# Optimization experiments

Measured on AMD Instinct MI355X. Metric: run time of the kernel, lower is better.

## Reference

```python
import jax, jax.numpy as jnp
import numpy as np

B, L, H, C = 1, 512, 1024, 2


def setup_inputs() -> dict:
    key = jax.random.key(0)
    k1, k2, k3 = jax.random.split(key, 3)
    lm_output = jax.random.normal(k1, (B, L, H), dtype=jnp.float32)
    # torch Linear weight layout: [out_features, in_features]
    W1 = jax.random.normal(k2, (H, 2 * H), dtype=jnp.float32) * 0.02
    b1 = jnp.zeros((H,), dtype=jnp.float32)
    W2 = jax.random.normal(k3, (C, H), dtype=jnp.float32) * 0.02
    b2 = jnp.zeros((C,), dtype=jnp.float32)
    return {"lm_output": lm_output, "W1": W1, "b1": b1, "W2": W2, "b2": b2}


def reference(lm_output, W1, b1, W2, b2):
    # pair_emb[b,i,j] = concat(lm_output[b,j], lm_output[b,i])
    # Linear(concat(a,b)) decomposes: split W1 into the halves acting on each part.
    Wa = W1[:, :H]  # acts on lm_output_a (the j / column token)
    Wb = W1[:, H:]  # acts on lm_output_b (the i / row token)
    a_proj = jnp.einsum('blh,oh->blo', lm_output, Wa)  # [B,L,H]
    b_proj = jnp.einsum('blh,oh->blo', lm_output, Wb)  # [B,L,H]
    # hidden[b,i,j] = tanh(a_proj[b,j] + b_proj[b,i] + b1)   -> [B,L,L,H]
    hidden = jnp.tanh(a_proj[:, None, :, :] + b_proj[:, :, None, :] + b1)
    # Dropout is identity at inference time.
    logits = jnp.einsum('bijh,ch->bijc', hidden, W2) + b2  # [B,L,L,C]
    logits = (logits + jnp.swapaxes(logits, 1, 2)) / 2.0
    return logits
```

## Files before the change

### kernel.cpp

```cpp
#include <hip/hip_runtime.h>
#include <hip/hip_bf16.h>

#define HH 1024
#define LL 512
#define TNT 8
#define NTILE 36

typedef __attribute__((ext_vector_type(8))) short bf16x8;
typedef __attribute__((ext_vector_type(4))) float f32x4;
typedef __attribute__((ext_vector_type(2))) float f32x2;

static constexpr float C_EXP = 2.8853900817779268f;

static __device__ __forceinline__ uint4 pack8(f32x4 a, f32x4 b) {
    union { uint4 u; __hip_bfloat162 h[4]; } r;
    r.h[0] = __float22bfloat162_rn(make_float2(a.x, a.y));
    r.h[1] = __float22bfloat162_rn(make_float2(a.z, a.w));
    r.h[2] = __float22bfloat162_rn(make_float2(b.x, b.y));
    r.h[3] = __float22bfloat162_rn(make_float2(b.z, b.w));
    return r.u;
}

static __device__ __forceinline__ f32x2 lo2(f32x4 v) { return __builtin_shufflevector(v, v, 0, 1); }
static __device__ __forceinline__ f32x2 hi2(f32x4 v) { return __builtin_shufflevector(v, v, 2, 3); }

__global__ __launch_bounds__(256, 4) void proj_mfma_kernel(
    const float* __restrict__ lm, const float* __restrict__ W1,
    const float* __restrict__ b1, float* __restrict__ Ea, float* __restrict__ Eb)
{
    __shared__ ushort As[64][136];
    __shared__ ushort Bs[32][136];

    const int tid  = threadIdx.x;
    const int lane = tid & 63;
    const int w    = tid >> 6;
    const int b    = blockIdx.x;
    const int xcd  = b & 7;
    const int idx  = b >> 3;
    const int nbase = (xcd * 8 + (idx & 7)) * 32;
    const int mbase = (idx >> 3) * 64;
    const int wm   = w * 16;
    const int sel  = nbase >> 10;
    const int nrow = nbase & 1023;

    const int frow = lane & 15;
    const int q8   = (lane >> 4) * 8;

    f32x4 acc[2] = {};

    for (int kb = 0; kb < HH; kb += 128) {
        __syncthreads();
        {
            int p = tid;
#pragma unroll
            for (int it = 0; it < 4; ++it, p += 256) {
                const int row = p >> 4, c8 = (p & 15) * 8;
                const float* pa = &lm[(mbase + row) * HH + kb + c8];
                *(uint4*)&As[row][c8] = pack8(*(const f32x4*)pa, *(const f32x4*)(pa + 4));
            }
            int q = tid;
#pragma unroll
            for (int it = 0; it < 2; ++it, q += 256) {
                const int row = q >> 4, c8 = (q & 15) * 8;
                const float* pw = &W1[(nrow + row) * 2048 + sel * 1024 + kb + c8];
                *(uint4*)&Bs[row][c8] = pack8(*(const f32x4*)pw, *(const f32x4*)(pw + 4));
            }
        }
        __syncthreads();

#pragma unroll
        for (int s = 0; s < 4; ++s) {
            const bf16x8 a = *(const bf16x8*)&As[wm + frow][s * 32 + q8];
#pragma unroll
            for (int nf = 0; nf < 2; ++nf) {
                const bf16x8 bb = *(const bf16x8*)&Bs[nf * 16 + frow][s * 32 + q8];
                acc[nf] = __builtin_amdgcn_mfma_f32_16x16x32_bf16(a, bb, acc[nf], 0, 0, 0);
            }
        }
    }

    const int col = lane & 15;
    const int rq  = (lane >> 4) * 4;
    const int m0  = mbase + wm + rq;
    const bool isA = sel == 0;
#pragma unroll
    for (int nf = 0; nf < 2; ++nf) {
        const int nn = (nrow + nf * 16 + col);
        if (isA) {
            const float bb = b1[nn];
#pragma unroll
            for (int r = 0; r < 4; ++r)
                Ea[(m0 + r) * HH + nn] = __builtin_amdgcn_exp2f(C_EXP * (acc[nf][r] + bb));
        } else {
#pragma unroll
            for (int r = 0; r < 4; ++r)
                Eb[(m0 + r) * HH + nn] = __builtin_amdgcn_exp2f(C_EXP * acc[nf][r]);
        }
    }
}

__global__ __launch_bounds__(256, 3) void pair_kernel(
    const float* __restrict__ Ea, const float* __restrict__ Eb,
    const float* __restrict__ W2, float* __restrict__ pbuf, int slice)
{
    __shared__ float tl[4][64][32];

    const int tid = threadIdx.x;
    const int tx  = tid & 15;
    const int ty  = tid >> 4;

    int tt = blockIdx.x, bi = 0, rem = TNT;
    while (tt >= rem) { tt -= rem; --rem; ++bi; }
    const int bj    = bi + tt;
    const int ibase = bi * 64;
    const int jbase = bj * 64;
    const int k0    = blockIdx.y * slice;

    f32x2 acc0[4][4] = {};
    f32x2 acc1[4][4] = {};
    const f32x2 one2 = {1.f, 1.f};

    for (int kb = 0; kb < slice; kb += 32) {
        if (kb) __syncthreads();
        {
            const int c4  = tid & 7;
            const int r0  = tid >> 3;
            const int hof = k0 + kb + c4 * 4;
#pragma unroll
            for (int it = 0; it < 8; ++it) {
                const int tile = it >> 1;
                const int row  = (it & 1) * 32 + r0;
                const int base = (tile < 2) ? jbase : ibase;
                const float* src = (tile == 0 || tile == 2) ? Ea : Eb;
                const int c4s = c4 ^ (row & 7);
                *(f32x4*)&tl[tile][row][c4s * 4] =
                    *(const f32x4*)&src[(size_t)(base + row) * HH + hof];
            }
        }
        __syncthreads();

#pragma unroll 1
        for (int h4 = 0; h4 < 8; ++h4) {
            const int sxj = (h4 ^ (tx & 7)) * 4;
            const int sxi = (h4 ^ (ty & 7)) * 4;

            f32x2 ailo[4], aihi[4], bilo[4], bihi[4];
#pragma unroll
            for (int ii = 0; ii < 4; ++ii) {
                const f32x4 Ai = *(const f32x4*)&tl[2][ty + 16 * ii][sxi];
                const f32x4 Bi = *(const f32x4*)&tl[3][ty + 16 * ii][sxi];
                ailo[ii] = lo2(Ai); aihi[ii] = hi2(Ai);
                bilo[ii] = lo2(Bi); bihi[ii] = hi2(Bi);
            }
            const f32x4 w0q = *(const f32x4*)&W2[k0 + kb + h4 * 4];
            const f32x4 w1q = *(const f32x4*)&W2[HH + k0 + kb + h4 * 4];
            const f32x2 w0lo = lo2(w0q), w0hi = hi2(w0q);
            const f32x2 w1lo = lo2(w1q), w1hi = hi2(w1q);

#pragma unroll
            for (int jj = 0; jj < 4; ++jj) {
                const f32x4 Aj = *(const f32x4*)&tl[0][tx + 16 * jj][sxj];
                const f32x4 Bj = *(const f32x4*)&tl[1][tx + 16 * jj][sxj];
                const f32x2 ajlo = lo2(Aj), ajhi = hi2(Aj);
                const f32x2 bjlo = lo2(Bj), bjhi = hi2(Bj);
#pragma unroll
                for (int ii = 0; ii < 4; ++ii) {
                    const f32x2 d01 = __builtin_elementwise_fma(bilo[ii], ajlo, one2);
                    const f32x2 d23 = __builtin_elementwise_fma(bihi[ii], ajhi, one2);
                    const f32x2 e01 = __builtin_elementwise_fma(ailo[ii], bjlo, one2);
                    const f32x2 e23 = __builtin_elementwise_fma(aihi[ii], bjhi, one2);
                    const f32x2 n01 = d01 + e01, n23 = d23 + e23;
                    const f32x2 m01 = d01 * e01, m23 = d23 * e23;
                    const float p01 = m01.x * m01.y;
                    const float p23 = m23.x * m23.y;
                    const float R   = __builtin_amdgcn_rcpf(p01 * p23);
                    const float r01 = R * p23;
                    const float r23 = R * p01;
                    const f32x2 u01 = (n01 * __builtin_shufflevector(m01, m01, 1, 0))
                                      * (f32x2){r01, r01};
                    const f32x2 u23 = (n23 * __builtin_shufflevector(m23, m23, 1, 0))
                                      * (f32x2){r23, r23};
                    acc0[ii][jj] = __builtin_elementwise_fma(u01, w0lo, acc0[ii][jj]);
                    acc0[ii][jj] = __builtin_elementwise_fma(u23, w0hi, acc0[ii][jj]);
                    acc1[ii][jj] = __builtin_elementwise_fma(u01, w1lo, acc1[ii][jj]);
                    acc1[ii][jj] = __builtin_elementwise_fma(u23, w1hi, acc1[ii][jj]);
                }
            }
        }
    }

    float* pb = pbuf + ((size_t)blockIdx.y * NTILE + blockIdx.x) * 8192;
#pragma unroll
    for (int ii = 0; ii < 4; ++ii)
#pragma unroll
        for (int jj = 0; jj < 4; ++jj) {
            const int li = ty + 16 * ii, lj = tx + 16 * jj;
            const f32x2 v = { acc0[ii][jj].x + acc0[ii][jj].y,
                              acc1[ii][jj].x + acc1[ii][jj].y };
            *(f32x2*)&pb[(li * 64 + lj) * 2] = v;
        }
}

__global__ __launch_bounds__(256) void combine_kernel(
    const float* __restrict__ pbuf, const float* __restrict__ W2,
    const float* __restrict__ b2, float* __restrict__ out, int nz)
{
    __shared__ float s_ws[2];

    const int tid = threadIdx.x;
    if (tid < 128) {
        const int c = tid >> 6, l = tid & 63;
        float s = 0.f;
#pragma unroll
        for (int q = 0; q < 4; ++q) {
            const f32x4 v = *(const f32x4*)&W2[c * HH + (l + q * 64) * 4];
            s += v.x + v.y + v.z + v.w;
        }
#pragma unroll
        for (int off = 32; off; off >>= 1) s += __shfl_down(s, off, 64);
        if (l == 0) s_ws[c] = s + b2[c];
    }
    __syncthreads();

    const int idx   = blockIdx.x * 256 + tid;
    const int t     = idx >> 13;
    const int local = idx & 8191;
    int tt = t, bi = 0, rem = TNT;
    while (tt >= rem) { tt -= rem; --rem; ++bi; }
    const int bj = bi + tt;

    float s0 = 0.f, s1 = 0.f, s2 = 0.f, s3 = 0.f;
    for (int z = 0; z < nz; z += 4) {
        s0 += pbuf[((size_t)z * NTILE + t) * 8192 + local];
        s1 += pbuf[((size_t)(z + 1) * NTILE + t) * 8192 + local];
        s2 += pbuf[((size_t)(z + 2) * NTILE + t) * 8192 + local];
        s3 += pbuf[((size_t)(z + 3) * NTILE + t) * 8192 + local];
    }
    const float s = (s0 + s1) + (s2 + s3);

    const int li = local >> 7;
    const int lj = (local >> 1) & 63;
    const int c  = local & 1;
    const float v = s_ws[c] - s;

    const int i = bi * 64 + li;
    const int j = bj * 64 + lj;
    out[(i * LL + j) * 2 + c] = v;
    out[(j * LL + i) * 2 + c] = v;
}

extern "C" void kernel_launch(void* const* d_in, const int* in_sizes, int n_in,
                              void* d_out, int out_size, void* d_ws, size_t ws_size,
                              hipStream_t stream)
{
    const float* lm = (const float*)d_in[0];
    const float* W1 = (const float*)d_in[1];
    const float* b1 = (const float*)d_in[2];
    const float* W2 = (const float*)d_in[3];
    const float* b2 = (const float*)d_in[4];
    float* out = (float*)d_out;

    char* ws = (char*)d_ws;
    float* Ea   = (float*)ws;
    float* Eb   = (float*)(ws + (2u << 20));
    float* pbuf = (float*)(ws + (4u << 20) + 64);

    const size_t ubase = (4u << 20) + 64;
    const size_t per_z = (size_t)NTILE * 8192 * 4;
    int nz = 8;
    if      (ws_size >= ubase + 32 * per_z) nz = 32;
    else if (ws_size >= ubase + 16 * per_z) nz = 16;
    const int slice = HH / nz;

    proj_mfma_kernel<<<512, 256, 0, stream>>>(lm, W1, b1, Ea, Eb);
    pair_kernel<<<dim3(NTILE, nz), 256, 0, stream>>>(Ea, Eb, W2, pbuf, slice);
    combine_kernel<<<(NTILE * 8192) / 256, 256, 0, stream>>>(pbuf, W2, b2, out, nz);
}
```

Baseline: 129.0 us.

## Shrink projection tiles, prefetch next K-slice into registers, unroll pair loop

The projection GEMM now uses 32x32 output tiles with four waves each owning one 16x16 MFMA tile, and the grid doubles to 1024 blocks to raise parallelism. Global loads for the next K-slice are issued into registers before the MFMA loop runs, so load latency overlaps compute. The pair kernel's inner h4 loop goes from unroll 1 to unroll 2. The costs are more register use and less reuse of each loaded tile.

Result: no change. 129.2 us (+0.2%).

```diff
diff --git a/kernel.cpp b/kernel.cpp
--- a/kernel.cpp
+++ b/kernel.cpp
@@ -28,7 +28,7 @@
     const float* __restrict__ lm, const float* __restrict__ W1,
     const float* __restrict__ b1, float* __restrict__ Ea, float* __restrict__ Eb)
 {
-    __shared__ ushort As[64][136];
+    __shared__ ushort As[32][136];
     __shared__ ushort Bs[32][136];
 
     const int tid  = threadIdx.x;
@@ -38,64 +38,71 @@
     const int xcd  = b & 7;
     const int idx  = b >> 3;
     const int nbase = (xcd * 8 + (idx & 7)) * 32;
-    const int mbase = (idx >> 3) * 64;
-    const int wm   = w * 16;
+    const int mbase = (idx >> 3) * 32;
+    const int wm   = (w & 1) * 16;
+    const int wn   = (w >> 1) * 16;
     const int sel  = nbase >> 10;
     const int nrow = nbase & 1023;
 
     const int frow = lane & 15;
     const int q8   = (lane >> 4) * 8;
 
-    f32x4 acc[2] = {};
-
+    const int r0a = tid >> 4;
+    const int c8  = (tid & 15) * 8;
+
+    f32x4 acc = {};
+    f32x4 ld[4][2];
+
+#define PLOAD(kb)                                                              \
+    {                                                                          \
+        const float* pa0 = &lm[(mbase + r0a) * HH + (kb) + c8];                \
+        const float* pa1 = &lm[(mbase + r0a + 16) * HH + (kb) + c8];           \
+        const float* pb0 = &W1[(nrow + r0a) * 2048 + sel * 1024 + (kb) + c8];  \
+        const float* pb1 = &W1[(nrow + r0a + 16) * 2048 + sel * 1024 + (kb) + c8]; \
+        ld[0][0] = *(const f32x4*)pa0; ld[0][1] = *(const f32x4*)(pa0 + 4);    \
+        ld[1][0] = *(const f32x4*)pa1; ld[1][1] = *(const f32x4*)(pa1 + 4);    \
+        ld[2][0] = *(const f32x4*)pb0; ld[2][1] = *(const f32x4*)(pb0 + 4);    \
+        ld[3][0] = *(const f32x4*)pb1; ld[3][1] = *(const f32x4*)(pb1 + 4);    \
+    }
+
+#define PSTORE()                                                               \
+    {                                                                          \
+        *(uint4*)&As[r0a][c8]      = pack8(ld[0][0], ld[0][1]);                \
+        *(uint4*)&As[r0a + 16][c8] = pack8(ld[1][0], ld[1][1]);                \
+        *(uint4*)&Bs[r0a][c8]      = pack8(ld[2][0], ld[2][1]);                \
+        *(uint4*)&Bs[r0a + 16][c8] = pack8(ld[3][0], ld[3][1]);                \
+    }
+
+    PLOAD(0)
     for (int kb = 0; kb < HH; kb += 128) {
         __syncthreads();
-        {
-            int p = tid;
-#pragma unroll
-            for (int it = 0; it < 4; ++it, p += 256) {
-                const int row = p >> 4, c8 = (p & 15) * 8;
-                const float* pa = &lm[(mbase + row) * HH + kb + c8];
-                *(uint4*)&As[row][c8] = pack8(*(const f32x4*)pa, *(const f32x4*)(pa + 4));
-            }
-            int q = tid;
-#pragma unroll
-            for (int it = 0; it < 2; ++it, q += 256) {
-                const int row = q >> 4, c8 = (q & 15) * 8;
-                const float* pw = &W1[(nrow + row) * 2048 + sel * 1024 + kb + c8];
-                *(uint4*)&Bs[row][c8] = pack8(*(const f32x4*)pw, *(const f32x4*)(pw + 4));
-            }
-        }
+        PSTORE()
+        if (kb + 128 < HH) PLOAD(kb + 128)
         __syncthreads();
 
 #pragma unroll
         for (int s = 0; s < 4; ++s) {
-            const bf16x8 a = *(const bf16x8*)&As[wm + frow][s * 32 + q8];
-#pragma unroll
-            for (int nf = 0; nf < 2; ++nf) {
-                const bf16x8 bb = *(const bf16x8*)&Bs[nf * 16 + frow][s * 32 + q8];
-                acc[nf] = __builtin_amdgcn_mfma_f32_16x16x32_bf16(a, bb, acc[nf], 0, 0, 0);
-            }
-        }
-    }
+            const bf16x8 a  = *(const bf16x8*)&As[wm + frow][s * 32 + q8];
+            const bf16x8 bb = *(const bf16x8*)&Bs[wn + frow][s * 32 + q8];
+            acc = __builtin_amdgcn_mfma_f32_16x16x32_bf16(a, bb, acc, 0, 0, 0);
+        }
+    }
+#undef PSTORE
+#undef PLOAD
 
     const int col = lane & 15;
     const int rq  = (lane >> 4) * 4;
     const int m0  = mbase + wm + rq;
-    const bool isA = sel == 0;
-#pragma unroll
-    for (int nf = 0; nf < 2; ++nf) {
-        const int nn = (nrow + nf * 16 + col);
-        if (isA) {
-            const float bb = b1[nn];
-#pragma unroll
-            for (int r = 0; r < 4; ++r)
-                Ea[(m0 + r) * HH + nn] = __builtin_amdgcn_exp2f(C_EXP * (acc[nf][r] + bb));
-        } else {
-#pragma unroll
-            for (int r = 0; r < 4; ++r)
-                Eb[(m0 + r) * HH + nn] = __builtin_amdgcn_exp2f(C_EXP * acc[nf][r]);
-        }
+    const int nn  = nrow + wn + col;
+    if (sel == 0) {
+        const float bb = b1[nn];
+#pragma unroll
+        for (int r = 0; r < 4; ++r)
+            Ea[(m0 + r) * HH + nn] = __builtin_amdgcn_exp2f(C_EXP * (acc[r] + bb));
+    } else {
+#pragma unroll
+        for (int r = 0; r < 4; ++r)
+            Eb[(m0 + r) * HH + nn] = __builtin_amdgcn_exp2f(C_EXP * acc[r]);
     }
 }
 
@@ -139,7 +146,7 @@
         }
         __syncthreads();
 
-#pragma unroll 1
+#pragma unroll 2
         for (int h4 = 0; h4 < 8; ++h4) {
             const int sxj = (h4 ^ (tx & 7)) * 4;
             const int sxi = (h4 ^ (ty & 7)) * 4;
@@ -272,7 +279,7 @@
     else if (ws_size >= ubase + 16 * per_z) nz = 16;
     const int slice = HH / nz;
 
-    proj_mfma_kernel<<<512, 256, 0, stream>>>(lm, W1, b1, Ea, Eb);
+    proj_mfma_kernel<<<1024, 256, 0, stream>>>(lm, W1, b1, Ea, Eb);
     pair_kernel<<<dim3(NTILE, nz), 256, 0, stream>>>(Ea, Eb, W2, pbuf, slice);
     combine_kernel<<<(NTILE * 8192) / 256, 256, 0, stream>>>(pbuf, W2, b2, out, nz);
 }
```
